# Performance work log

Hardware: AMD Instinct MI355X
Metric: run time of the kernel (lower is better)

## Reference

```python
import jax, jax.numpy as jnp
import numpy as np

HH = 38  # sqrt(amd0=1444)
KD = 3   # 3x3 neighborhood


def setup_inputs() -> dict:
    key = jax.random.key(0)
    fm = jax.random.normal(key, (16, 512, HH, HH), dtype=jnp.float32)
    return {"fm": fm}


def reference(fm):
    # fm: [B, C, H, W] -> replication pad 1 -> NHWC -> gather 3x3 neighbors,
    # concatenated along the channel axis in row-major neighbor order
    # (matching counts[:, 0..8] = (h-1,w-1),(h-1,w),(h-1,w+1),(h,w-1),...).
    B, C, H, W = fm.shape
    x = jnp.pad(fm, ((0, 0), (0, 0), (1, 1), (1, 1)), mode="edge")  # [B,C,H+2,W+2]
    x = jnp.transpose(x, (0, 2, 3, 1))  # [B, H+2, W+2, C]
    patches = [x[:, di:di + H, dj:dj + W, :] for di in range(KD) for dj in range(KD)]
    pfm = jnp.concatenate(patches, axis=-1)  # [B, H, W, 9*C]
    return pfm.reshape(B, H * W, KD * KD * C)  # [B, 1444, 9*C]
```

## Files before the change

### kernel.cpp

```cpp
#include <hip/hip_runtime.h>


#define BB 16
#define CC 512
#define HH 38
#define WW 38
#define HW (HH * WW)
#define KK 9
#define NT 256
#define CG 32
#define HC 5

typedef float f32x2 __attribute__((ext_vector_type(2)));
typedef float f32x4 __attribute__((ext_vector_type(4)));

__global__ __launch_bounds__(NT) void spatial_pool_closure(
    const float* __restrict__ fm, float* __restrict__ out)
{
    const unsigned L = blockIdx.x;
    const int hc  = (int)(L & 7u);
    const int cgb = (int)((L >> 3) & 15u);
    const int b   = (int)(L >> 7);

    const int R0 = hc * HC;
    const int NR = (hc == 7) ? (HH - R0) : HC;
    const int NP = NR * 19;

    const int t  = (int)threadIdx.x;
    const int c4 = t & 7;
    const int pp = t >> 3;

    const int c0 = cgb * CG + 4 * c4;
    const float* pl0 = fm + (size_t)(b * CC + c0) * HW;
    float* ob = out + c0;
    const int obase = b * HW;

    for (int p = pp; p < NP; p += 32) {
        const int lr  = p / 19;
        const int wp  = p - lr * 19;
        const int h   = R0 + lr;
        const int w0  = 2 * wp;

        const size_t ro = (size_t)h * WW + w0;
        const f32x2 t0 = *(const f32x2*)(pl0 + (size_t)0 * HW + ro);
        const f32x2 t1 = *(const f32x2*)(pl0 + (size_t)1 * HW + ro);
        const f32x2 t2 = *(const f32x2*)(pl0 + (size_t)2 * HW + ro);
        const f32x2 t3 = *(const f32x2*)(pl0 + (size_t)3 * HW + ro);
        const f32x4 va = (f32x4){t0.x, t1.x, t2.x, t3.x};
        const f32x4 vb = (f32x4){t0.y, t1.y, t2.y, t3.y};

        const int hr0 = (h < HH - 1) ? (obase + (h + 1) * WW) * KK + 0
                                     : (obase + (HH - 1) * WW) * KK + 6;
        const int hr1 = (obase + h * WW) * KK + 3;
        const int hr2 = (h > 0) ? (obase + (h - 1) * WW) * KK + 6
                                : (obase) * KK + 0;

        #pragma unroll
        for (int par = 0; par < 2; ++par) {
            const int w = w0 + par;
            const f32x4 val = par ? vb : va;
            const int wo0 = (w < WW - 1) ? (w + 1) * KK + 0 : (WW - 1) * KK + 2;
            const int wo1 = w * KK + 1;
            const int wo2 = (w > 0) ? (w - 1) * KK + 2 : 0;
            const int wt[3] = { wo0, wo1, wo2 };
            const int ht[3] = { hr0, hr1, hr2 };

            #pragma unroll
            for (int i = 0; i < 3; ++i) {
                #pragma unroll
                for (int j = 0; j < 3; ++j) {
                    const unsigned idx = (unsigned)(ht[i] + wt[j]) * (unsigned)CC;
                    __builtin_nontemporal_store(val, (f32x4*)(ob + (size_t)idx));
                }
            }
        }
    }
}

extern "C" void kernel_launch(void* const* d_in, const int* in_sizes, int n_in,
                              void* d_out, int out_size, void* d_ws, size_t ws_size,
                              hipStream_t stream) {
    const float* fm = (const float*)d_in[0];
    float* out = (float*)d_out;
    dim3 grid(BB * (CC / CG) * 8);
    dim3 block(NT);
    spatial_pool_closure<<<grid, block, 0, stream>>>(fm, out);
}
```

Before: 456.9 us.

## Transpose one image row per block through LDS and write output rows contiguously

Each block now handles one batch, one image row and half the channels. It loads the row from all 256 channel planes into a padded LDS tile, transposing NCHW to WC. Each wave then reads neighbor columns from LDS and writes whole contiguous 1 KB channel spans of output, instead of scattered 16-byte stores from 4-channel groups. This aims for fully coalesced output writes, at the cost of an LDS transpose, a barrier and somewhat uncoalesced strided input loads.

```diff
diff --git a/kernel.cpp b/kernel.cpp
--- a/kernel.cpp
+++ b/kernel.cpp
@@ -8,70 +8,63 @@
 #define HW (HH * WW)
 #define KK 9
 #define NT 256
-#define CG 32
-#define HC 5
+#define PD 260
 
 typedef float f32x2 __attribute__((ext_vector_type(2)));
 typedef float f32x4 __attribute__((ext_vector_type(4)));
 
-__global__ __launch_bounds__(NT) void spatial_pool_closure(
+__global__ __launch_bounds__(NT) void spatial_pool_lds(
     const float* __restrict__ fm, float* __restrict__ out)
 {
+    __shared__ float T[WW][PD];
+
     const unsigned L = blockIdx.x;
-    const int hc  = (int)(L & 7u);
-    const int cgb = (int)((L >> 3) & 15u);
-    const int b   = (int)(L >> 7);
+    const int b    = (int)(L & 15u);
+    const int rest = (int)(L >> 4);
+    const int h    = rest >> 1;
+    const int half = rest & 1;
 
-    const int R0 = hc * HC;
-    const int NR = (hc == 7) ? (HH - R0) : HC;
-    const int NP = NR * 19;
+    const int tid = (int)threadIdx.x;
 
-    const int t  = (int)threadIdx.x;
-    const int c4 = t & 7;
-    const int pp = t >> 3;
+    const f32x2* s2 = (const f32x2*)(fm + (size_t)(b * CC + half * 256) * HW);
+    const unsigned hbase = (unsigned)h * 19u;
+    #pragma unroll
+    for (int r = 0; r < 19; ++r) {
+        const unsigned task = (unsigned)(r * 256 + tid);
+        const unsigned c = task / 19u;
+        const unsigned j = task - 19u * c;
+        const f32x2 v = s2[c * 722u + hbase + j];
+        T[2 * j + 0][c] = v.x;
+        T[2 * j + 1][c] = v.y;
+    }
+    __syncthreads();
 
-    const int c0 = cgb * CG + 4 * c4;
-    const float* pl0 = fm + (size_t)(b * CC + c0) * HW;
-    float* ob = out + c0;
     const int obase = b * HW;
+    const int hr0 = (h < HH - 1) ? (obase + (h + 1) * WW) * KK + 0
+                                 : (obase + (HH - 1) * WW) * KK + 6;
+    const int hr1 = (obase + h * WW) * KK + 3;
+    const int hr2 = (h > 0) ? (obase + (h - 1) * WW) * KK + 6
+                            : obase * KK + 0;
+    const int ht[3] = { hr0, hr1, hr2 };
 
-    for (int p = pp; p < NP; p += 32) {
-        const int lr  = p / 19;
-        const int wp  = p - lr * 19;
-        const int h   = R0 + lr;
-        const int w0  = 2 * wp;
+    const int wv = tid >> 6;
+    const int l  = tid & 63;
+    float* ob = out + half * 256 + 4 * l;
 
-        const size_t ro = (size_t)h * WW + w0;
-        const f32x2 t0 = *(const f32x2*)(pl0 + (size_t)0 * HW + ro);
-        const f32x2 t1 = *(const f32x2*)(pl0 + (size_t)1 * HW + ro);
-        const f32x2 t2 = *(const f32x2*)(pl0 + (size_t)2 * HW + ro);
-        const f32x2 t3 = *(const f32x2*)(pl0 + (size_t)3 * HW + ro);
-        const f32x4 va = (f32x4){t0.x, t1.x, t2.x, t3.x};
-        const f32x4 vb = (f32x4){t0.y, t1.y, t2.y, t3.y};
-
-        const int hr0 = (h < HH - 1) ? (obase + (h + 1) * WW) * KK + 0
-                                     : (obase + (HH - 1) * WW) * KK + 6;
-        const int hr1 = (obase + h * WW) * KK + 3;
-        const int hr2 = (h > 0) ? (obase + (h - 1) * WW) * KK + 6
-                                : (obase) * KK + 0;
-
+    for (int wp = wv; wp < WW; wp += 4) {
+        const int wm = (wp > 0) ? wp - 1 : 0;
+        const int wq = (wp < WW - 1) ? wp + 1 : WW - 1;
+        f32x4 vv[3];
+        vv[0] = *(const f32x4*)&T[wm][4 * l];
+        vv[1] = *(const f32x4*)&T[wp][4 * l];
+        vv[2] = *(const f32x4*)&T[wq][4 * l];
         #pragma unroll
-        for (int par = 0; par < 2; ++par) {
-            const int w = w0 + par;
-            const f32x4 val = par ? vb : va;
-            const int wo0 = (w < WW - 1) ? (w + 1) * KK + 0 : (WW - 1) * KK + 2;
-            const int wo1 = w * KK + 1;
-            const int wo2 = (w > 0) ? (w - 1) * KK + 2 : 0;
-            const int wt[3] = { wo0, wo1, wo2 };
-            const int ht[3] = { hr0, hr1, hr2 };
-
+        for (int i = 0; i < 3; ++i) {
+            const size_t base = (size_t)(unsigned)(ht[i] + wp * KK) * (size_t)CC;
             #pragma unroll
-            for (int i = 0; i < 3; ++i) {
-                #pragma unroll
-                for (int j = 0; j < 3; ++j) {
-                    const unsigned idx = (unsigned)(ht[i] + wt[j]) * (unsigned)CC;
-                    __builtin_nontemporal_store(val, (f32x4*)(ob + (size_t)idx));
-                }
+            for (int dj = 0; dj < 3; ++dj) {
+                __builtin_nontemporal_store(vv[dj],
+                    (f32x4*)(ob + base + (size_t)dj * CC));
             }
         }
     }
@@ -82,7 +75,7 @@
                               hipStream_t stream) {
     const float* fm = (const float*)d_in[0];
     float* out = (float*)d_out;
-    dim3 grid(BB * (CC / CG) * 8);
+    dim3 grid(BB * HH * 2);
     dim3 block(NT);
-    spatial_pool_closure<<<grid, block, 0, stream>>>(fm, out);
+    spatial_pool_lds<<<grid, block, 0, stream>>>(fm, out);
 }
```

Result: no change. 451.0 us (-1.3%).
